# Optimization experiments

Hardware: AMD Instinct MI355X
Metric: run time of the kernel (lower is better)

## Reference

```python
import jax, jax.numpy as jnp
import numpy as np

SEQ, B, I, H = 2048, 64, 512, 512

def setup_inputs() -> dict:
    key = jax.random.key(0)
    k1, k2, k3, k4, k5 = jax.random.split(key, 5)
    s = 1.0 / np.sqrt(H)  # torch LSTMCell init: U(-1/sqrt(H), 1/sqrt(H))
    return {
        "input_seq": jax.random.normal(k1, (SEQ, B, I), dtype=jnp.float32),
        "W_ih": jax.random.uniform(k2, (4 * H, I), minval=-s, maxval=s, dtype=jnp.float32),
        "W_hh": jax.random.uniform(k3, (4 * H, H), minval=-s, maxval=s, dtype=jnp.float32),
        "b_ih": jax.random.uniform(k4, (4 * H,), minval=-s, maxval=s, dtype=jnp.float32),
        "b_hh": jax.random.uniform(k5, (4 * H,), minval=-s, maxval=s, dtype=jnp.float32),
    }

def reference(input_seq, W_ih, W_hh, b_ih, b_hh):
    # Precompute input projections for all timesteps in one big matmul.
    # x_proj: (seq, B, 4H)
    x_proj = jnp.einsum('sbi,gi->sbg', input_seq, W_ih) + b_ih + b_hh
    B_ = input_seq.shape[1]
    Hh = W_hh.shape[1]

    def step(carry, xp):
        h, c = carry
        gates = xp + h @ W_hh.T  # (B, 4H)
        i, f, g, o = jnp.split(gates, 4, axis=-1)  # torch gate order i,f,g,o
        i = jax.nn.sigmoid(i)
        f = jax.nn.sigmoid(f)
        g = jnp.tanh(g)
        o = jax.nn.sigmoid(o)
        c_new = f * c + i * g
        h_new = o * jnp.tanh(c_new)
        return (h_new, c_new), h_new

    h0 = jnp.zeros((B_, Hh), dtype=input_seq.dtype)
    c0 = jnp.zeros((B_, Hh), dtype=input_seq.dtype)
    (h_n, c_n), outputs = jax.lax.scan(step, (h0, c0), x_proj)
    return outputs, h_n, c_n
```

## Files before the change

kernel.cpp:

```cpp
#include <hip/hip_runtime.h>
#include <stdint.h>


typedef __bf16 bf16;
typedef __bf16 bf16x4 __attribute__((ext_vector_type(4)));
typedef __bf16 bf16x8 __attribute__((ext_vector_type(8)));
typedef float  f32x4  __attribute__((ext_vector_type(4)));

#define SEQN  2048
#define BATCH 64
#define IDIM  512
#define HDIM  512
#define GDIM  2048
#define NTOT  131072

#define CNT_OFF  0u
#define H0_OFF   1024u
#define H1_OFF   (H0_OFF + 65536u)
#define BIAS_OFF (H1_OFF + 65536u)
#define WIH_OFF  (BIAS_OFF + 8192u)
#define WHH_OFF  (WIH_OFF + 2097152u)
#define XBF_OFF  (WHH_OFF + 2097152u)
#define XP_OFF   (XBF_OFF + 134217728u)

__device__ __forceinline__ float sigf(float x)     { return 1.0f / (1.0f + __expf(-x)); }
__device__ __forceinline__ float tanhfast(float x) { return 2.0f / (1.0f + __expf(-2.0f * x)) - 1.0f; }

__global__ void k_init(const float* __restrict__ bih, const float* __restrict__ bhh,
                       float* __restrict__ bias, uint32_t* __restrict__ zbase, int zwords) {
    int i = blockIdx.x * blockDim.x + threadIdx.x;
    int stride = gridDim.x * blockDim.x;
    for (int j = i; j < zwords; j += stride) zbase[j] = 0u;
    for (int j = i; j < GDIM;   j += stride) bias[j] = bih[j] + bhh[j];
}

__global__ void k_cvt(const float* __restrict__ in, bf16* __restrict__ out, int n4) {
    int stride = gridDim.x * blockDim.x;
    for (int j = blockIdx.x * blockDim.x + threadIdx.x; j < n4; j += stride) {
        float4 v = ((const float4*)in)[j];
        bf16x4 o;
        o[0] = (bf16)v.x; o[1] = (bf16)v.y; o[2] = (bf16)v.z; o[3] = (bf16)v.w;
        *((bf16x4*)out + j) = o;
    }
}

__global__ __launch_bounds__(256) void k_gemm_xproj(const bf16* __restrict__ Wb,
                                                    const bf16* __restrict__ Xb,
                                                    const float* __restrict__ bias,
                                                    bf16* __restrict__ xp) {
    __shared__ bf16 As[128 * 72];
    __shared__ bf16 Bs[128 * 72];
    const int tid = threadIdx.x;
    const int bm = blockIdx.x, bn = blockIdx.y;
    const int w = tid >> 6, lane = tid & 63;
    const int l15 = lane & 15, quad = lane >> 4;
    const int mh = (w >> 1) << 6, nh = (w & 1) << 6;

    f32x4 acc[4][4];
#pragma unroll
    for (int i = 0; i < 4; ++i)
#pragma unroll
        for (int j = 0; j < 4; ++j) { f32x4 z = {0.f, 0.f, 0.f, 0.f}; acc[i][j] = z; }

    for (int kk = 0; kk < 512; kk += 64) {
#pragma unroll
        for (int it = 0; it < 4; ++it) {
            int off  = it * 4096 + tid * 16;
            int row  = off >> 7;
            int colh = (off & 127) >> 1;
            *(bf16x8*)(&As[row * 72 + colh]) =
                *(const bf16x8*)(Wb + (size_t)(bm * 128 + row) * 512 + kk + colh);
            *(bf16x8*)(&Bs[row * 72 + colh]) =
                *(const bf16x8*)(Xb + (size_t)(bn * 128 + row) * 512 + kk + colh);
        }
        __syncthreads();
#pragma unroll
        for (int ks = 0; ks < 2; ++ks) {
            bf16x8 af[4], bfm[4];
#pragma unroll
            for (int mt = 0; mt < 4; ++mt)
                af[mt]  = *(const bf16x8*)(&As[(mh + mt * 16 + l15) * 72 + ks * 32 + quad * 8]);
#pragma unroll
            for (int nt = 0; nt < 4; ++nt)
                bfm[nt] = *(const bf16x8*)(&Bs[(nh + nt * 16 + l15) * 72 + ks * 32 + quad * 8]);
#pragma unroll
            for (int mt = 0; mt < 4; ++mt)
#pragma unroll
                for (int nt = 0; nt < 4; ++nt)
                    acc[mt][nt] = __builtin_amdgcn_mfma_f32_16x16x32_bf16(af[mt], bfm[nt], acc[mt][nt], 0, 0, 0);
        }
        __syncthreads();
    }

#pragma unroll
    for (int mt = 0; mt < 4; ++mt)
#pragma unroll
        for (int r = 0; r < 4; ++r) {
            int g = bm * 128 + mh + mt * 16 + quad * 4 + r;
            float bv = bias[g];
#pragma unroll
            for (int nt = 0; nt < 4; ++nt) {
                int n = bn * 128 + nh + nt * 16 + l15;
                xp[(size_t)g * NTOT + n] = (bf16)(acc[mt][nt][r] + bv);
            }
        }
}

__global__ __launch_bounds__(256, 1) void k_lstm(const bf16* __restrict__ Whh,
                                                 const bf16* __restrict__ xp,
                                                 bf16* h0, bf16* h1, int* cnt,
                                                 float* __restrict__ out) {
    const int tid = threadIdx.x;
    const int w = tid >> 6, lane = tid & 63;
    const int l15 = lane & 15, quad = lane >> 4;
    const int u0 = blockIdx.x << 4;
    const int b  = (w << 4) + l15;

    bf16x8 a[4][16];
#pragma unroll
    for (int mt = 0; mt < 4; ++mt) {
        const bf16* wrow = Whh + (size_t)(mt * 512 + u0 + l15) * 512 + quad * 8;
#pragma unroll
        for (int kt = 0; kt < 16; ++kt) a[mt][kt] = *(const bf16x8*)(wrow + kt * 32);
    }

    float cc[4] = {0.f, 0.f, 0.f, 0.f};

    for (int t = 0; t < SEQN; ++t) {
        const bf16* hr = (t & 1) ? h1 : h0;
        bf16*       hw = (t & 1) ? h0 : h1;

        bf16x8 bfr[16];
        const bf16* hrow = hr + b * 512 + quad * 8;
#pragma unroll
        for (int kt = 0; kt < 16; ++kt) bfr[kt] = *(const bf16x8*)(hrow + kt * 32);

        f32x4 acc[4];
#pragma unroll
        for (int mt = 0; mt < 4; ++mt) {
            const bf16* xrow = xp + (size_t)(mt * 512 + u0 + quad * 4) * NTOT + t * 64 + b;
            f32x4 v;
#pragma unroll
            for (int r = 0; r < 4; ++r) v[r] = (float)xrow[(size_t)r * NTOT];
            acc[mt] = v;
        }

#pragma unroll
        for (int kt = 0; kt < 16; ++kt)
#pragma unroll
            for (int mt = 0; mt < 4; ++mt)
                acc[mt] = __builtin_amdgcn_mfma_f32_16x16x32_bf16(a[mt][kt], bfr[kt], acc[mt], 0, 0, 0);

        float hv[4];
#pragma unroll
        for (int r = 0; r < 4; ++r) {
            float iv = sigf(acc[0][r]);
            float fv = sigf(acc[1][r]);
            float gv = tanhfast(acc[2][r]);
            float ov = sigf(acc[3][r]);
            cc[r] = fv * cc[r] + iv * gv;
            hv[r] = ov * tanhfast(cc[r]);
        }

        const int u = u0 + (quad << 2);
        float4 o4 = make_float4(hv[0], hv[1], hv[2], hv[3]);
        *(float4*)(out + (size_t)t * 32768 + b * 512 + u) = o4;
        bf16x4 h4;
        h4[0] = (bf16)hv[0]; h4[1] = (bf16)hv[1]; h4[2] = (bf16)hv[2]; h4[3] = (bf16)hv[3];
        *(bf16x4*)(hw + b * 512 + u) = h4;

        if (t == SEQN - 1) {
            *(float4*)(out + (size_t)SEQN * 32768 + b * 512 + u) = o4;
            float4 c4 = make_float4(cc[0], cc[1], cc[2], cc[3]);
            *(float4*)(out + (size_t)SEQN * 32768 + 32768 + b * 512 + u) = c4;
        } else {
            __syncthreads();
            if (tid == 0) {
                __threadfence();
                __hip_atomic_fetch_add(cnt, 1, __ATOMIC_ACQ_REL, __HIP_MEMORY_SCOPE_AGENT);
                const int target = (t + 1) * 32;
                while (__hip_atomic_load(cnt, __ATOMIC_ACQUIRE, __HIP_MEMORY_SCOPE_AGENT) < target)
                    __builtin_amdgcn_s_sleep(2);
            }
            __syncthreads();
            __builtin_amdgcn_fence(__ATOMIC_ACQUIRE, "agent");
        }
    }
}

extern "C" void kernel_launch(void* const* d_in, const int* in_sizes, int n_in,
                              void* d_out, int out_size, void* d_ws, size_t ws_size,
                              hipStream_t stream) {
    (void)in_sizes; (void)n_in; (void)out_size; (void)ws_size;
    const float* X   = (const float*)d_in[0];
    const float* Wih = (const float*)d_in[1];
    const float* Whh = (const float*)d_in[2];
    const float* bih = (const float*)d_in[3];
    const float* bhh = (const float*)d_in[4];
    float* out = (float*)d_out;
    char*  ws  = (char*)d_ws;

    float* bias = (float*)(ws + BIAS_OFF);
    bf16*  Wihb = (bf16*)(ws + WIH_OFF);
    bf16*  Whhb = (bf16*)(ws + WHH_OFF);
    bf16*  Xb   = (bf16*)(ws + XBF_OFF);
    bf16*  xp   = (bf16*)(ws + XP_OFF);
    bf16*  h0   = (bf16*)(ws + H0_OFF);
    bf16*  h1   = (bf16*)(ws + H1_OFF);
    int*   cnt  = (int*)(ws + CNT_OFF);

    k_init<<<64, 256, 0, stream>>>(bih, bhh, bias, (uint32_t*)ws, (int)(BIAS_OFF / 4));
    k_cvt<<<8192, 256, 0, stream>>>(X,   Xb,   NTOT * IDIM / 4);
    k_cvt<<<1024, 256, 0, stream>>>(Wih, Wihb, GDIM * IDIM / 4);
    k_cvt<<<1024, 256, 0, stream>>>(Whh, Whhb, GDIM * HDIM / 4);
    dim3 gg(16, 1024);
    k_gemm_xproj<<<gg, 256, 0, stream>>>(Wihb, Xb, bias, xp);
    k_lstm<<<32, 256, 0, stream>>>(Whhb, xp, h0, h1, cnt, out);
}
```

Baseline: 16.62 ms.

## Replace atomic-counter grid barrier with per-block flags and prefetch next x projection

Swaps the single shared atomic counter with fence-heavy acquire/release spinning for per-block flag words on separate cache lines. Each wave polls all 32 flags in parallel using relaxed agent-scope atomics and a wave vote. The hidden-state reads and writes become relaxed agent-scope atomics so they bypass stale caches without full fences. The next timestep's input-projection values are prefetched before the barrier so their latency overlaps the wait. The cost is relying on relaxed ordering plus a hand-written s_waitcnt/s_barrier for correctness, which is fragile if the compiler reorders the stores.

```diff
diff --git a/kernel.cpp b/kernel.cpp
--- a/kernel.cpp
+++ b/kernel.cpp
@@ -6,6 +6,7 @@
 typedef __bf16 bf16x4 __attribute__((ext_vector_type(4)));
 typedef __bf16 bf16x8 __attribute__((ext_vector_type(8)));
 typedef float  f32x4  __attribute__((ext_vector_type(4)));
+typedef unsigned long long u64;
 
 #define SEQN  2048
 #define BATCH 64
@@ -13,6 +14,7 @@
 #define HDIM  512
 #define GDIM  2048
 #define NTOT  131072
+#define NBLK  32
 
 #define CNT_OFF  0u
 #define H0_OFF   1024u
@@ -108,7 +110,7 @@
 
 __global__ __launch_bounds__(256, 1) void k_lstm(const bf16* __restrict__ Whh,
                                                  const bf16* __restrict__ xp,
-                                                 bf16* h0, bf16* h1, int* cnt,
+                                                 bf16* h0, bf16* h1, uint32_t* flags,
                                                  float* __restrict__ out) {
     const int tid = threadIdx.x;
     const int w = tid >> 6, lane = tid & 63;
@@ -126,23 +128,33 @@
 
     float cc[4] = {0.f, 0.f, 0.f, 0.f};
 
+    bf16 xn[4][4];
+#pragma unroll
+    for (int mt = 0; mt < 4; ++mt) {
+        const bf16* xrow = xp + (size_t)(mt * 512 + u0 + (quad << 2)) * NTOT + b;
+#pragma unroll
+        for (int r = 0; r < 4; ++r) xn[mt][r] = xrow[(size_t)r * NTOT];
+    }
+
     for (int t = 0; t < SEQN; ++t) {
         const bf16* hr = (t & 1) ? h1 : h0;
         bf16*       hw = (t & 1) ? h0 : h1;
 
         bf16x8 bfr[16];
-        const bf16* hrow = hr + b * 512 + quad * 8;
-#pragma unroll
-        for (int kt = 0; kt < 16; ++kt) bfr[kt] = *(const bf16x8*)(hrow + kt * 32);
+        const u64* hq = (const u64*)(hr + b * 512 + quad * 8);
+#pragma unroll
+        for (int kt = 0; kt < 16; ++kt) {
+            u64 q0 = __hip_atomic_load(hq + kt * 8,     __ATOMIC_RELAXED, __HIP_MEMORY_SCOPE_AGENT);
+            u64 q1 = __hip_atomic_load(hq + kt * 8 + 1, __ATOMIC_RELAXED, __HIP_MEMORY_SCOPE_AGENT);
+            union { u64 q[2]; bf16x8 v; } uu; uu.q[0] = q0; uu.q[1] = q1;
+            bfr[kt] = uu.v;
+        }
 
         f32x4 acc[4];
 #pragma unroll
         for (int mt = 0; mt < 4; ++mt) {
-            const bf16* xrow = xp + (size_t)(mt * 512 + u0 + quad * 4) * NTOT + t * 64 + b;
-            f32x4 v;
-#pragma unroll
-            for (int r = 0; r < 4; ++r) v[r] = (float)xrow[(size_t)r * NTOT];
-            acc[mt] = v;
+#pragma unroll
+            for (int r = 0; r < 4; ++r) acc[mt][r] = (float)xn[mt][r];
         }
 
 #pragma unroll
@@ -167,23 +179,35 @@
         *(float4*)(out + (size_t)t * 32768 + b * 512 + u) = o4;
         bf16x4 h4;
         h4[0] = (bf16)hv[0]; h4[1] = (bf16)hv[1]; h4[2] = (bf16)hv[2]; h4[3] = (bf16)hv[3];
-        *(bf16x4*)(hw + b * 512 + u) = h4;
+        union { bf16x4 v; u64 q; } hu; hu.v = h4;
+        __hip_atomic_store((u64*)(hw + b * 512 + u), hu.q, __ATOMIC_RELAXED, __HIP_MEMORY_SCOPE_AGENT);
 
         if (t == SEQN - 1) {
             *(float4*)(out + (size_t)SEQN * 32768 + b * 512 + u) = o4;
             float4 c4 = make_float4(cc[0], cc[1], cc[2], cc[3]);
             *(float4*)(out + (size_t)SEQN * 32768 + 32768 + b * 512 + u) = c4;
         } else {
-            __syncthreads();
-            if (tid == 0) {
-                __threadfence();
-                __hip_atomic_fetch_add(cnt, 1, __ATOMIC_ACQ_REL, __HIP_MEMORY_SCOPE_AGENT);
-                const int target = (t + 1) * 32;
-                while (__hip_atomic_load(cnt, __ATOMIC_ACQUIRE, __HIP_MEMORY_SCOPE_AGENT) < target)
-                    __builtin_amdgcn_s_sleep(2);
+            asm volatile("" ::: "memory");
+#pragma unroll
+            for (int mt = 0; mt < 4; ++mt) {
+                const bf16* xrow = xp + (size_t)(mt * 512 + u0 + (quad << 2)) * NTOT
+                                      + (size_t)(t + 1) * 64 + b;
+#pragma unroll
+                for (int r = 0; r < 4; ++r) xn[mt][r] = xrow[(size_t)r * NTOT];
             }
-            __syncthreads();
-            __builtin_amdgcn_fence(__ATOMIC_ACQUIRE, "agent");
+            asm volatile("s_waitcnt vmcnt(16)" ::: "memory");
+            asm volatile("s_barrier" ::: "memory");
+            if (tid == 0)
+                __hip_atomic_store(flags + (blockIdx.x << 3), (uint32_t)(t + 1),
+                                   __ATOMIC_RELAXED, __HIP_MEMORY_SCOPE_AGENT);
+            const uint32_t tgt = (uint32_t)(t + 1);
+            for (;;) {
+                uint32_t fv = __hip_atomic_load(flags + ((lane & 31) << 3),
+                                                __ATOMIC_RELAXED, __HIP_MEMORY_SCOPE_AGENT);
+                if (__all((int)(fv >= tgt))) break;
+                __builtin_amdgcn_s_sleep(1);
+            }
+            asm volatile("" ::: "memory");
         }
     }
 }
@@ -207,7 +231,7 @@
     bf16*  xp   = (bf16*)(ws + XP_OFF);
     bf16*  h0   = (bf16*)(ws + H0_OFF);
     bf16*  h1   = (bf16*)(ws + H1_OFF);
-    int*   cnt  = (int*)(ws + CNT_OFF);
+    uint32_t* flags = (uint32_t*)(ws + CNT_OFF);
 
     k_init<<<64, 256, 0, stream>>>(bih, bhh, bias, (uint32_t*)ws, (int)(BIAS_OFF / 4));
     k_cvt<<<8192, 256, 0, stream>>>(X,   Xb,   NTOT * IDIM / 4);
@@ -215,5 +239,5 @@
     k_cvt<<<1024, 256, 0, stream>>>(Whh, Whhb, GDIM * HDIM / 4);
     dim3 gg(16, 1024);
     k_gemm_xproj<<<gg, 256, 0, stream>>>(Wihb, Xb, bias, xp);
-    k_lstm<<<32, 256, 0, stream>>>(Whhb, xp, h0, h1, cnt, out);
-}
+    k_lstm<<<32, 256, 0, stream>>>(Whhb, xp, h0, h1, flags, out);
+}
```

Result: faster. 13.91 ms (-16.3%).
